# Kernel tuning notes

Measured on AMD Instinct MI355X. Metric: run time of the kernel, lower is better.

The kernel has to match this reference:

```python
import jax, jax.numpy as jnp
import numpy as np

N_HEAD = 16    # config.n_head
T_STEPS = 3    # config.T: PC energy-minimization steps
LR = 0.01      # config.local_learning_rate


def _causal_attention(x, Wq, Wk, Wv):
    # x: [B, S, E] latent activity; generative model f(x) = causal MHA(x)
    B, S, E = x.shape
    D = E // N_HEAD
    def split(h):  # [B,S,E] -> [B,H,S,D]
        return h.reshape(B, S, N_HEAD, D).transpose(0, 2, 1, 3)
    q = split(x @ Wq.T)
    k = split(x @ Wk.T)
    v = split(x @ Wv.T)
    scores = jnp.einsum('bhqd,bhkd->bhqk', q, k) / jnp.sqrt(jnp.asarray(D, x.dtype))
    mask = jnp.tril(jnp.ones((S, S), dtype=bool))
    scores = jnp.where(mask, scores, jnp.asarray(-1e30, x.dtype))
    att = jax.nn.softmax(scores, axis=-1)
    out = jnp.einsum('bhqk,bhkd->bhqd', att, v)
    return out.transpose(0, 2, 1, 3).reshape(B, S, E)


def _pc_infer(target, f):
    # PCLayer: T steps of gradient descent on E(x) = 0.5 * ||target - f(x)||^2
    # x_init = 'zeros'; returns the inferred latent x (PCLayer.get_x).
    x = jnp.zeros_like(target)
    energy = lambda z: 0.5 * jnp.sum((target - f(z)) ** 2)
    g = jax.grad(energy)
    for _ in range(T_STEPS):  # fixed small T: unrolled
        x = x - LR * g(x)
    return x


def setup_inputs() -> dict:
    key = jax.random.key(0)
    ks = jax.random.split(key, 5)
    B, S, E = 2, 1024, 1024
    fc1_x = jax.random.normal(ks[0], (B, S, E), dtype=jnp.float32)
    init = lambda k: 0.02 * jax.random.normal(k, (E, E), dtype=jnp.float32)
    return {
        'fc1_x': fc1_x,
        'Wq': init(ks[1]),
        'Wk': init(ks[2]),
        'Wv': init(ks[3]),
        'Wo': init(ks[4]),
    }


def reference(fc1_x, Wq, Wk, Wv, Wo):
    # Stage 1 (pc_output): infer pre-output latent att_score s.t. output-proj
    # Wo @ att_score ~ fc1_x  (generative model f1(x) = x @ Wo^T, bias=False).
    att_score = _pc_infer(fc1_x, lambda z: z @ Wo.T)
    # Stage 2 (pc_qkv): infer latent x_qkv s.t. causal MHA(x_qkv) ~ att_score.
    x_qkv = _pc_infer(att_score, lambda z: _causal_attention(z, Wq, Wk, Wv))
    return x_qkv
```

## Files before the change

kernel.cpp:

```cpp
#include <hip/hip_runtime.h>
#include <hip/hip_bf16.h>
#include <math.h>

#define S_LEN 1024
#define E_DIM 1024
#define NH 16
#define HD 64
#define M_ROWS 2048
#define BH_CNT 32

static constexpr float LR_C = 0.01f;
static constexpr float SC_C = 0.125f;
static constexpr float C2_C = 0.125f * 1.44269504f;

typedef unsigned short ushort_t;
typedef __attribute__((ext_vector_type(8))) __bf16 bf16x8;
typedef __attribute__((ext_vector_type(4))) float f32x4;

static __device__ inline ushort_t f2bu(float f) {
  __hip_bfloat16 h = __float2bfloat16(f);
  return *(ushort_t*)&h;
}
static __device__ inline bf16x8 ldg8(const ushort_t* p) { return *(const bf16x8*)p; }

static __device__ inline void async_cp16(const ushort_t* g, __bf16* lds_wave_base) {
  __builtin_amdgcn_global_load_lds((const __attribute__((address_space(1))) void*)g,
                                   (__attribute__((address_space(3))) void*)lds_wave_base,
                                   16, 0, 0);
}

static __device__ inline void stage_tile(const ushort_t* src, size_t src_stride,
                                         ushort_t* lds, int lane, int wave) {
  int rl = lane >> 3;
  int c = ((lane & 7) - rl) & 7;
  #pragma unroll
  for (int t = 0; t < 2; t++) {
    int s = wave * 2 + t;
    async_cp16(src + (size_t)(s * 8 + rl) * src_stride + c * 8,
               (__bf16*)(lds + s * 512));
  }
}
static __device__ inline const bf16x8* tile_at(const ushort_t* lds, int r, int cchunk) {
  return (const bf16x8*)(lds + r * 64 + (((cchunk + r) & 7) * 8));
}

__global__ __launch_bounds__(256) void prep_w4(
    const float* __restrict__ Wo, const float* __restrict__ Wq,
    const float* __restrict__ Wk, const float* __restrict__ Wv,
    ushort_t* __restrict__ o0, ushort_t* __restrict__ t0,
    ushort_t* __restrict__ o1, ushort_t* __restrict__ t1,
    ushort_t* __restrict__ o2, ushort_t* __restrict__ t2,
    ushort_t* __restrict__ o3, ushort_t* __restrict__ t3) {
  __shared__ float ts[64][65];
  int z = blockIdx.z;
  const float* W = (z == 0) ? Wo : (z == 1) ? Wq : (z == 2) ? Wk : Wv;
  ushort_t* Wb  = (z == 0) ? o0 : (z == 1) ? o1 : (z == 2) ? o2 : o3;
  ushort_t* WTb = (z == 0) ? t0 : (z == 1) ? t1 : (z == 2) ? t2 : t3;
  int bx = blockIdx.x * 64, by = blockIdx.y * 64;
  int t = threadIdx.x;
  int rr = t >> 6, cc = t & 63;
  #pragma unroll
  for (int p = 0; p < 16; p++) {
    int r = p * 4 + rr;
    float v = W[(size_t)(by + r) * E_DIM + bx + cc];
    ts[r][cc] = v;
    Wb[(size_t)(by + r) * E_DIM + bx + cc] = f2bu(v);
  }
  __syncthreads();
  #pragma unroll
  for (int p = 0; p < 16; p++) {
    int r = p * 4 + rr;
    WTb[(size_t)(bx + r) * E_DIM + by + cc] = f2bu(ts[cc][r]);
  }
}

__global__ __launch_bounds__(256) void k_cast(const float* __restrict__ in,
                                              ushort_t* __restrict__ out, int n4) {
  int i = blockIdx.x * 256 + threadIdx.x;
  if (i < n4) {
    float4 v = ((const float4*)in)[i];
    ushort_t p[4] = {f2bu(v.x), f2bu(v.y), f2bu(v.z), f2bu(v.w)};
    *(uint2*)(out + (size_t)i * 4) = *(uint2*)p;
  }
}

__global__ __launch_bounds__(256) void k_scan1(const float* __restrict__ Xs,
                                               float* __restrict__ Sf,
                                               float* __restrict__ tot) {
  int e = blockIdx.x * 256 + threadIdx.x;
  int b = blockIdx.y;
  int z = blockIdx.z;
  float acc = 0.f;
  for (int i = z * 64 + 63; i >= z * 64; i--) {
    size_t idx = ((size_t)b * S_LEN + i) * E_DIM + e;
    acc = fmaf(Xs[idx], 1.0f / (float)(i + 1), acc);
    Sf[idx] = acc;
  }
  tot[((size_t)b * 16 + z) * E_DIM + e] = acc;
}

__global__ __launch_bounds__(256) void k_scan2(const float* __restrict__ Sf,
                                               const float* __restrict__ tot,
                                               ushort_t* __restrict__ Sb) {
  int e = blockIdx.x * 256 + threadIdx.x;
  int b = blockIdx.y;
  int z = blockIdx.z;
  float off = 0.f;
  for (int c = z + 1; c < 16; c++) off += tot[((size_t)b * 16 + c) * E_DIM + e];
  for (int i = z * 64; i < z * 64 + 64; i++) {
    size_t idx = ((size_t)b * S_LEN + i) * E_DIM + e;
    Sb[idx] = f2bu(Sf[idx] + off);
  }
}

template <int MODE>
__global__ __launch_bounds__(256) void gemm_mf(
    const ushort_t* __restrict__ A, const ushort_t* __restrict__ B,
    float* __restrict__ Cf, ushort_t* __restrict__ Cb0, float alpha) {
  const int K = 1024;
  __shared__ __bf16 As[2][2][64][32];
  __shared__ __bf16 Bs[2][2][64][32];
  int tid = threadIdx.x;
  int m0 = blockIdx.y * 64, n0 = blockIdx.x * 64;

  int lane = tid & 63, wave = tid >> 6;
  int wrow = wave >> 1, wcol = wave & 1;
  int fr = lane & 15, q = lane >> 4;

  int srow = wave * 16 + (lane >> 2);
  int scg = ((lane & 3) + (srow >> 1)) & 3;
  int scol = scg * 8;

  int rA0 = wrow * 32 + fr, rA1r = rA0 + 16;
  int rB0 = wcol * 32 + fr, rB1r = rB0 + 16;
  int cA0 = ((q - (rA0 >> 1)) & 3) * 8;
  int cA1 = ((q - (rA1r >> 1)) & 3) * 8;
  int cB0 = ((q - (rB0 >> 1)) & 3) * 8;
  int cB1 = ((q - (rB1r >> 1)) & 3) * 8;

  const ushort_t* ga = A + (size_t)(m0 + srow) * K + scol;
  const ushort_t* gb = B + (size_t)(n0 + srow) * K + scol;

  f32x4 acc[2][2] = {};

  async_cp16(ga,      &As[0][0][wave * 16][0]);
  async_cp16(ga + 32, &As[0][1][wave * 16][0]);
  async_cp16(gb,      &Bs[0][0][wave * 16][0]);
  async_cp16(gb + 32, &Bs[0][1][wave * 16][0]);

  #pragma unroll 1
  for (int k0 = 0; k0 < K; k0 += 64) {
    int cur = (k0 >> 6) & 1;
    __syncthreads();
    if (k0 + 64 < K) {
      int nxt = cur ^ 1;
      async_cp16(ga + k0 + 64, &As[nxt][0][wave * 16][0]);
      async_cp16(ga + k0 + 96, &As[nxt][1][wave * 16][0]);
      async_cp16(gb + k0 + 64, &Bs[nxt][0][wave * 16][0]);
      async_cp16(gb + k0 + 96, &Bs[nxt][1][wave * 16][0]);
    }
    bf16x8 a00 = *(const bf16x8*)&As[cur][0][rA0][cA0];
    bf16x8 a01 = *(const bf16x8*)&As[cur][1][rA0][cA0];
    bf16x8 a10 = *(const bf16x8*)&As[cur][0][rA1r][cA1];
    bf16x8 a11 = *(const bf16x8*)&As[cur][1][rA1r][cA1];
    bf16x8 b00 = *(const bf16x8*)&Bs[cur][0][rB0][cB0];
    bf16x8 b01 = *(const bf16x8*)&Bs[cur][1][rB0][cB0];
    bf16x8 b10 = *(const bf16x8*)&Bs[cur][0][rB1r][cB1];
    bf16x8 b11 = *(const bf16x8*)&Bs[cur][1][rB1r][cB1];
    acc[0][0] = __builtin_amdgcn_mfma_f32_16x16x32_bf16(a00, b00, acc[0][0], 0, 0, 0);
    acc[0][1] = __builtin_amdgcn_mfma_f32_16x16x32_bf16(a00, b10, acc[0][1], 0, 0, 0);
    acc[1][0] = __builtin_amdgcn_mfma_f32_16x16x32_bf16(a10, b00, acc[1][0], 0, 0, 0);
    acc[1][1] = __builtin_amdgcn_mfma_f32_16x16x32_bf16(a10, b10, acc[1][1], 0, 0, 0);
    acc[0][0] = __builtin_amdgcn_mfma_f32_16x16x32_bf16(a01, b01, acc[0][0], 0, 0, 0);
    acc[0][1] = __builtin_amdgcn_mfma_f32_16x16x32_bf16(a01, b11, acc[0][1], 0, 0, 0);
    acc[1][0] = __builtin_amdgcn_mfma_f32_16x16x32_bf16(a11, b01, acc[1][0], 0, 0, 0);
    acc[1][1] = __builtin_amdgcn_mfma_f32_16x16x32_bf16(a11, b11, acc[1][1], 0, 0, 0);
  }

  #pragma unroll
  for (int mi = 0; mi < 2; mi++)
    #pragma unroll
    for (int ni = 0; ni < 2; ni++) {
      int col = n0 + wcol * 32 + ni * 16 + fr;
      int row0 = m0 + wrow * 32 + mi * 16 + q * 4;
      #pragma unroll
      for (int r = 0; r < 4; r++) {
        size_t idx = (size_t)(row0 + r) * E_DIM + col;
        float v = acc[mi][ni][r];
        if (MODE == 3) {
          Cf[idx] = v;
        } else if (MODE == 4) {
          Cf[idx] = v;
          Cb0[idx] = f2bu(v);
        } else if (MODE == 6) {
          float nv = alpha * v;
          Cf[idx] = nv;
          Cb0[idx] = f2bu(nv);
        } else if (MODE == 7) {
          float nv = -3.f * LR_C * LR_C * Cf[idx] + LR_C * LR_C * LR_C * v;
          if (row0 + r == col) nv += 3.f * LR_C;
          Cb0[idx] = f2bu(nv);
        } else {
          Cb0[idx] = f2bu(v);
        }
      }
    }
}

__global__ __launch_bounds__(256) void gemm_qkv(
    const ushort_t* __restrict__ A,
    const ushort_t* __restrict__ B0, const ushort_t* __restrict__ B1, const ushort_t* __restrict__ B2,
    ushort_t* __restrict__ Cb0, ushort_t* __restrict__ Cb1, ushort_t* __restrict__ Cb2,
    ushort_t* __restrict__ Ct0, ushort_t* __restrict__ Ct1, ushort_t* __restrict__ Ct2) {
  const int K = 1024;
  __shared__ __bf16 As[2][2][64][32];
  __shared__ __bf16 Bs[2][3][2][64][32];
  int tid = threadIdx.x;
  int m0 = blockIdx.y * 64, n0 = blockIdx.x * 64;

  int lane = tid & 63, wave = tid >> 6;
  int wrow = wave >> 1, wcol = wave & 1;
  int fr = lane & 15, q = lane >> 4;

  int srow = wave * 16 + (lane >> 2);
  int scg = ((lane & 3) + (srow >> 1)) & 3;
  int scol = scg * 8;

  int rA0 = wrow * 32 + fr, rA1r = rA0 + 16;
  int rB0 = wcol * 32 + fr, rB1r = rB0 + 16;
  int cA0 = ((q - (rA0 >> 1)) & 3) * 8;
  int cA1 = ((q - (rA1r >> 1)) & 3) * 8;
  int cB0 = ((q - (rB0 >> 1)) & 3) * 8;
  int cB1 = ((q - (rB1r >> 1)) & 3) * 8;

  const ushort_t* ga = A + (size_t)(m0 + srow) * K + scol;
  const ushort_t* gb0 = B0 + (size_t)(n0 + srow) * K + scol;
  const ushort_t* gb1 = B1 + (size_t)(n0 + srow) * K + scol;
  const ushort_t* gb2 = B2 + (size_t)(n0 + srow) * K + scol;

  f32x4 acc[3][2][2] = {};

  async_cp16(ga,       &As[0][0][wave * 16][0]);
  async_cp16(ga + 32,  &As[0][1][wave * 16][0]);
  async_cp16(gb0,      &Bs[0][0][0][wave * 16][0]);
  async_cp16(gb0 + 32, &Bs[0][0][1][wave * 16][0]);
  async_cp16(gb1,      &Bs[0][1][0][wave * 16][0]);
  async_cp16(gb1 + 32, &Bs[0][1][1][wave * 16][0]);
  async_cp16(gb2,      &Bs[0][2][0][wave * 16][0]);
  async_cp16(gb2 + 32, &Bs[0][2][1][wave * 16][0]);

  #pragma unroll 1
  for (int k0 = 0; k0 < K; k0 += 64) {
    int cur = (k0 >> 6) & 1;
    __syncthreads();
    if (k0 + 64 < K) {
      int nxt = cur ^ 1;
      async_cp16(ga + k0 + 64,  &As[nxt][0][wave * 16][0]);
      async_cp16(ga + k0 + 96,  &As[nxt][1][wave * 16][0]);
      async_cp16(gb0 + k0 + 64, &Bs[nxt][0][0][wave * 16][0]);
      async_cp16(gb0 + k0 + 96, &Bs[nxt][0][1][wave * 16][0]);
      async_cp16(gb1 + k0 + 64, &Bs[nxt][1][0][wave * 16][0]);
      async_cp16(gb1 + k0 + 96, &Bs[nxt][1][1][wave * 16][0]);
      async_cp16(gb2 + k0 + 64, &Bs[nxt][2][0][wave * 16][0]);
      async_cp16(gb2 + k0 + 96, &Bs[nxt][2][1][wave * 16][0]);
    }
    bf16x8 a00 = *(const bf16x8*)&As[cur][0][rA0][cA0];
    bf16x8 a01 = *(const bf16x8*)&As[cur][1][rA0][cA0];
    bf16x8 a10 = *(const bf16x8*)&As[cur][0][rA1r][cA1];
    bf16x8 a11 = *(const bf16x8*)&As[cur][1][rA1r][cA1];
    #pragma unroll
    for (int z = 0; z < 3; z++) {
      bf16x8 b00 = *(const bf16x8*)&Bs[cur][z][0][rB0][cB0];
      bf16x8 b01 = *(const bf16x8*)&Bs[cur][z][1][rB0][cB0];
      bf16x8 b10 = *(const bf16x8*)&Bs[cur][z][0][rB1r][cB1];
      bf16x8 b11 = *(const bf16x8*)&Bs[cur][z][1][rB1r][cB1];
      acc[z][0][0] = __builtin_amdgcn_mfma_f32_16x16x32_bf16(a00, b00, acc[z][0][0], 0, 0, 0);
      acc[z][0][1] = __builtin_amdgcn_mfma_f32_16x16x32_bf16(a00, b10, acc[z][0][1], 0, 0, 0);
      acc[z][1][0] = __builtin_amdgcn_mfma_f32_16x16x32_bf16(a10, b00, acc[z][1][0], 0, 0, 0);
      acc[z][1][1] = __builtin_amdgcn_mfma_f32_16x16x32_bf16(a10, b10, acc[z][1][1], 0, 0, 0);
      acc[z][0][0] = __builtin_amdgcn_mfma_f32_16x16x32_bf16(a01, b01, acc[z][0][0], 0, 0, 0);
      acc[z][0][1] = __builtin_amdgcn_mfma_f32_16x16x32_bf16(a01, b11, acc[z][0][1], 0, 0, 0);
      acc[z][1][0] = __builtin_amdgcn_mfma_f32_16x16x32_bf16(a11, b01, acc[z][1][0], 0, 0, 0);
      acc[z][1][1] = __builtin_amdgcn_mfma_f32_16x16x32_bf16(a11, b11, acc[z][1][1], 0, 0, 0);
    }
  }

  #pragma unroll
  for (int z = 0; z < 3; z++) {
    ushort_t* Cbz = (z == 0) ? Cb0 : (z == 1) ? Cb1 : Cb2;
    ushort_t* Ctz = (z == 0) ? Ct0 : (z == 1) ? Ct1 : Ct2;
    float tsc = (z == 2) ? 1.0f : SC_C;
    #pragma unroll
    for (int mi = 0; mi < 2; mi++)
      #pragma unroll
      for (int ni = 0; ni < 2; ni++) {
        int col = n0 + wcol * 32 + ni * 16 + fr;
        int row0 = m0 + wrow * 32 + mi * 16 + q * 4;
        ushort_t pk[4];
        #pragma unroll
        for (int r = 0; r < 4; r++) {
          size_t idx = (size_t)(row0 + r) * E_DIM + col;
          float v = acc[z][mi][ni][r];
          Cbz[idx] = f2bu(v);
          pk[r] = f2bu(v * tsc);
        }
        int hh = col >> 6, dd = col & 63;
        int bb = row0 >> 10, ss = row0 & 1023;
        *(uint2*)(Ctz + ((size_t)((bb * NH + hh) * HD + dd)) * S_LEN + ss) = *(uint2*)pk;
      }
  }
}

__global__ __launch_bounds__(256) void gemm_acc(
    const ushort_t* __restrict__ A0, const ushort_t* __restrict__ A1, const ushort_t* __restrict__ A2,
    const ushort_t* __restrict__ B0, const ushort_t* __restrict__ B1, const ushort_t* __restrict__ B2,
    float* __restrict__ Cf, ushort_t* __restrict__ Cb, float alpha) {
  const int K = 1024;
  __shared__ __bf16 As[3][2][64][32];
  __shared__ __bf16 Bs[3][2][64][32];
  int tid = threadIdx.x;
  int m0 = blockIdx.y * 64, n0 = blockIdx.x * 64;

  int lane = tid & 63, wave = tid >> 6;
  int wrow = wave >> 1, wcol = wave & 1;
  int fr = lane & 15, q = lane >> 4;

  int srow = wave * 16 + (lane >> 2);
  int scg = ((lane & 3) + (srow >> 1)) & 3;
  int scol = scg * 8;

  int rA0 = wrow * 32 + fr, rA1r = rA0 + 16;
  int rB0 = wcol * 32 + fr, rB1r = rB0 + 16;
  int cA0 = ((q - (rA0 >> 1)) & 3) * 8;
  int cA1 = ((q - (rA1r >> 1)) & 3) * 8;
  int cB0 = ((q - (rB0 >> 1)) & 3) * 8;
  int cB1 = ((q - (rB1r >> 1)) & 3) * 8;

  f32x4 acc[3][2][2] = {};

  const ushort_t* ga0 = A0 + (size_t)(m0 + srow) * K + scol;
  const ushort_t* ga1 = A1 + (size_t)(m0 + srow) * K + scol;
  const ushort_t* ga2 = A2 + (size_t)(m0 + srow) * K + scol;
  const ushort_t* gb0 = B0 + (size_t)(n0 + srow) * K + scol;
  const ushort_t* gb1 = B1 + (size_t)(n0 + srow) * K + scol;
  const ushort_t* gb2 = B2 + (size_t)(n0 + srow) * K + scol;

  #pragma unroll 1
  for (int k0 = 0; k0 < K; k0 += 64) {
    __syncthreads();
    async_cp16(ga0 + k0,      &As[0][0][wave * 16][0]);
    async_cp16(ga0 + k0 + 32, &As[0][1][wave * 16][0]);
    async_cp16(ga1 + k0,      &As[1][0][wave * 16][0]);
    async_cp16(ga1 + k0 + 32, &As[1][1][wave * 16][0]);
    async_cp16(ga2 + k0,      &As[2][0][wave * 16][0]);
    async_cp16(ga2 + k0 + 32, &As[2][1][wave * 16][0]);
    async_cp16(gb0 + k0,      &Bs[0][0][wave * 16][0]);
    async_cp16(gb0 + k0 + 32, &Bs[0][1][wave * 16][0]);
    async_cp16(gb1 + k0,      &Bs[1][0][wave * 16][0]);
    async_cp16(gb1 + k0 + 32, &Bs[1][1][wave * 16][0]);
    async_cp16(gb2 + k0,      &Bs[2][0][wave * 16][0]);
    async_cp16(gb2 + k0 + 32, &Bs[2][1][wave * 16][0]);
    __syncthreads();
    #pragma unroll
    for (int z = 0; z < 3; z++) {
      bf16x8 a00 = *(const bf16x8*)&As[z][0][rA0][cA0];
      bf16x8 a01 = *(const bf16x8*)&As[z][1][rA0][cA0];
      bf16x8 a10 = *(const bf16x8*)&As[z][0][rA1r][cA1];
      bf16x8 a11 = *(const bf16x8*)&As[z][1][rA1r][cA1];
      bf16x8 b00 = *(const bf16x8*)&Bs[z][0][rB0][cB0];
      bf16x8 b01 = *(const bf16x8*)&Bs[z][1][rB0][cB0];
      bf16x8 b10 = *(const bf16x8*)&Bs[z][0][rB1r][cB1];
      bf16x8 b11 = *(const bf16x8*)&Bs[z][1][rB1r][cB1];
      acc[z][0][0] = __builtin_amdgcn_mfma_f32_16x16x32_bf16(a00, b00, acc[z][0][0], 0, 0, 0);
      acc[z][0][1] = __builtin_amdgcn_mfma_f32_16x16x32_bf16(a00, b10, acc[z][0][1], 0, 0, 0);
      acc[z][1][0] = __builtin_amdgcn_mfma_f32_16x16x32_bf16(a10, b00, acc[z][1][0], 0, 0, 0);
      acc[z][1][1] = __builtin_amdgcn_mfma_f32_16x16x32_bf16(a10, b10, acc[z][1][1], 0, 0, 0);
      acc[z][0][0] = __builtin_amdgcn_mfma_f32_16x16x32_bf16(a01, b01, acc[z][0][0], 0, 0, 0);
      acc[z][0][1] = __builtin_amdgcn_mfma_f32_16x16x32_bf16(a01, b11, acc[z][0][1], 0, 0, 0);
      acc[z][1][0] = __builtin_amdgcn_mfma_f32_16x16x32_bf16(a11, b01, acc[z][1][0], 0, 0, 0);
      acc[z][1][1] = __builtin_amdgcn_mfma_f32_16x16x32_bf16(a11, b11, acc[z][1][1], 0, 0, 0);
    }
  }

  #pragma unroll
  for (int mi = 0; mi < 2; mi++)
    #pragma unroll
    for (int ni = 0; ni < 2; ni++) {
      int col = n0 + wcol * 32 + ni * 16 + fr;
      int row0 = m0 + wrow * 32 + mi * 16 + q * 4;
      #pragma unroll
      for (int r = 0; r < 4; r++) {
        size_t idx = (size_t)(row0 + r) * E_DIM + col;
        float v = (acc[0][mi][ni][r] + acc[1][mi][ni][r]) + acc[2][mi][ni][r];
        float nv = Cf[idx] + alpha * v;
        Cf[idx] = nv;
        Cb[idx] = f2bu(nv);
      }
    }
}


__global__ __launch_bounds__(256) void fwd_fused(const ushort_t* __restrict__ Qg,
                                                 const ushort_t* __restrict__ Kg,
                                                 const ushort_t* __restrict__ Vt,
                                                 const float* __restrict__ Xs,
                                                 float* __restrict__ mbuf,
                                                 ushort_t* __restrict__ Gb,
                                                 ushort_t* __restrict__ Gt,
                                                 float* __restrict__ Dv) {
  int bh = blockIdx.x, y = blockIdx.y;
  int it = (y < 8) ? (15 - y) : (y - 8);
  int b = bh >> 4, h = bh & 15;
  int tid = threadIdx.x, lane = tid & 63, wv = tid >> 6;
  int fr = lane & 15, q = lane >> 4;
  int i0 = it * 64, band = wv * 16;
  __shared__ ushort_t Ksb[2][4096];
  __shared__ ushort_t Vsb[2][4096];
  __shared__ ushort_t Ps[64][72];

  const ushort_t* Kbase = Kg + (size_t)(b * S_LEN) * E_DIM + h * HD;
  const ushort_t* Vbase = Vt + (size_t)(bh * HD) * S_LEN;

  const ushort_t* Qrow = Qg + (size_t)(b * S_LEN + i0 + band + fr) * E_DIM + h * HD;
  bf16x8 aq0 = ldg8(Qrow + q * 8);
  bf16x8 aq1 = ldg8(Qrow + 32 + q * 8);

  float m[4], l[4];
  #pragma unroll
  for (int r = 0; r < 4; r++) { m[r] = -1e30f; l[r] = 0.f; }
  f32x4 oacc[4] = {};

  stage_tile(Kbase, E_DIM, Ksb[0], lane, wv);
  stage_tile(Vbase, S_LEN, Vsb[0], lane, wv);

  #pragma unroll 1
  for (int jt = 0; jt <= it; jt++) {
    int j0 = jt * 64;
    int cur = jt & 1;
    __syncthreads();
    if (jt < it) {
      int j0n = j0 + 64;
      stage_tile(Kbase + (size_t)j0n * E_DIM, E_DIM, Ksb[cur ^ 1], lane, wv);
      stage_tile(Vbase + j0n, S_LEN, Vsb[cur ^ 1], lane, wv);
    }
    const ushort_t* Ks = Ksb[cur];
    const ushort_t* Vs = Vsb[cur];
    f32x4 sA[4];
    #pragma unroll
    for (int nc = 0; nc < 4; nc++) {
      bf16x8 bk0 = *tile_at(Ks, nc * 16 + fr, q);
      bf16x8 bk1 = *tile_at(Ks, nc * 16 + fr, q + 4);
      f32x4 z = {};
      z = __builtin_amdgcn_mfma_f32_16x16x32_bf16(aq0, bk0, z, 0, 0, 0);
      sA[nc] = __builtin_amdgcn_mfma_f32_16x16x32_bf16(aq1, bk1, z, 0, 0, 0);
    }
    float sv[4][4];
    if (jt == it) {
      #pragma unroll
      for (int nc = 0; nc < 4; nc++)
        #pragma unroll
        for (int r = 0; r < 4; r++) {
          int row = i0 + band + q * 4 + r;
          int col = j0 + nc * 16 + fr;
          sv[nc][r] = (col <= row) ? sA[nc][r] * C2_C : -1e30f;
        }
    } else {
      #pragma unroll
      for (int nc = 0; nc < 4; nc++)
        #pragma unroll
        for (int r = 0; r < 4; r++)
          sv[nc][r] = sA[nc][r] * C2_C;
    }
    #pragma unroll
    for (int r = 0; r < 4; r++) {
      float mx = fmaxf(fmaxf(sv[0][r], sv[1][r]), fmaxf(sv[2][r], sv[3][r]));
      #pragma unroll
      for (int off = 1; off < 16; off <<= 1) mx = fmaxf(mx, __shfl_xor(mx, off, 64));
      float mn = fmaxf(m[r], mx);
      float alpha = exp2f(m[r] - mn);
      float ps = 0.f;
      #pragma unroll
      for (int nc = 0; nc < 4; nc++) {
        float p = exp2f(sv[nc][r] - mn);
        Ps[band + q * 4 + r][nc * 16 + fr] = f2bu(p);
        ps += p;
      }
      l[r] = l[r] * alpha + ps;
      m[r] = mn;
      #pragma unroll
      for (int nc = 0; nc < 4; nc++) oacc[nc][r] *= alpha;
    }
    bf16x8 ap0 = *(const bf16x8*)&Ps[band + fr][q * 8];
    bf16x8 ap1 = *(const bf16x8*)&Ps[band + fr][32 + q * 8];
    #pragma unroll
    for (int nc = 0; nc < 4; nc++) {
      bf16x8 bv0 = *tile_at(Vs, nc * 16 + fr, q);
      bf16x8 bv1 = *tile_at(Vs, nc * 16 + fr, q + 4);
      oacc[nc] = __builtin_amdgcn_mfma_f32_16x16x32_bf16(ap0, bv0, oacc[nc], 0, 0, 0);
      oacc[nc] = __builtin_amdgcn_mfma_f32_16x16x32_bf16(ap1, bv1, oacc[nc], 0, 0, 0);
    }
  }
  #pragma unroll
  for (int r = 0; r < 4; r++) {
    #pragma unroll
    for (int off = 1; off < 16; off <<= 1) l[r] += __shfl_xor(l[r], off, 64);
  }
  float linv[4];
  #pragma unroll
  for (int r = 0; r < 4; r++) linv[r] = 1.0f / l[r];
  float dpart[4] = {};
  #pragma unroll
  for (int nc = 0; nc < 4; nc++) {
    ushort_t pg[4];
    #pragma unroll
    for (int r = 0; r < 4; r++) {
      int row = i0 + band + q * 4 + r;
      size_t gi = (size_t)(b * S_LEN + row) * E_DIM + h * HD + nc * 16 + fr;
      float o = oacc[nc][r] * linv[r];
      float g = o - Xs[gi];
      ushort_t bu = f2bu(g);
      Gb[gi] = bu;
      pg[r] = bu;
      dpart[r] += g * o;
    }
    int d = nc * 16 + fr;
    int s0 = i0 + band + q * 4;
    *(uint2*)(Gt + ((size_t)bh * HD + d) * S_LEN + s0) = *(uint2*)pg;
  }
  #pragma unroll
  for (int r = 0; r < 4; r++) {
    #pragma unroll
    for (int off = 1; off < 16; off <<= 1) dpart[r] += __shfl_xor(dpart[r], off, 64);
  }
  if (fr == 0) {
    #pragma unroll
    for (int r = 0; r < 4; r++) {
      size_t sid = (size_t)bh * S_LEN + i0 + band + q * 4 + r;
      mbuf[sid] = m[r] + log2f(l[r]);
      Dv[sid] = dpart[r];
    }
  }
}

__global__ __launch_bounds__(256) void bwd_fused(const ushort_t* __restrict__ Qg,
                                                 const ushort_t* __restrict__ Kg,
                                                 const ushort_t* __restrict__ Vg,
                                                 const ushort_t* __restrict__ Gg,
                                                 const ushort_t* __restrict__ Qt,
                                                 const ushort_t* __restrict__ Kt,
                                                 const ushort_t* __restrict__ Gt,
                                                 const float* __restrict__ mbuf,
                                                 const float* __restrict__ Dv,
                                                 ushort_t* __restrict__ GQ,
                                                 ushort_t* __restrict__ GK,
                                                 ushort_t* __restrict__ GV) {
  int bh = blockIdx.x, y = blockIdx.y;
  int b = bh >> 4, h = bh & 15;
  int tid = threadIdx.x, lane = tid & 63, wv = tid >> 6;
  int fr = lane & 15, q = lane >> 4;
  int band = wv * 16;
  __shared__ ushort_t tA[4][4096];
  __shared__ ushort_t tP[2][64][72];

  {
    ushort_t* Ks = tA[0];
    ushort_t* Vs = tA[1];
    ushort_t* Ts = tA[2];
    ushort_t (*dSs)[72] = tP[0];
    int it = y, i0 = it * 64;

    const ushort_t* KbaseA = Kg + (size_t)(b * S_LEN) * E_DIM + h * HD;
    const ushort_t* VbaseA = Vg + (size_t)(b * S_LEN) * E_DIM + h * HD;
    const ushort_t* TbaseA = Kt + (size_t)(bh * HD) * S_LEN;

    const ushort_t* Qrow = Qg + (size_t)(b * S_LEN + i0 + band + fr) * E_DIM + h * HD;
    const ushort_t* Grow = Gg + (size_t)(b * S_LEN + i0 + band + fr) * E_DIM + h * HD;
    bf16x8 aq0 = ldg8(Qrow + q * 8), aq1 = ldg8(Qrow + 32 + q * 8);
    bf16x8 ag0 = ldg8(Grow + q * 8), ag1 = ldg8(Grow + 32 + q * 8);

    float mrow[4], Dr[4];
    #pragma unroll
    for (int r = 0; r < 4; r++) {
      size_t sid = (size_t)bh * S_LEN + i0 + band + q * 4 + r;
      mrow[r] = mbuf[sid]; Dr[r] = Dv[sid];
    }
    f32x4 dqacc[4] = {};

    #pragma unroll 1
    for (int jt = 0; jt <= it; jt++) {
      int j0 = jt * 64;
      __syncthreads();
      stage_tile(KbaseA + (size_t)j0 * E_DIM, E_DIM, Ks, lane, wv);
      stage_tile(VbaseA + (size_t)j0 * E_DIM, E_DIM, Vs, lane, wv);
      stage_tile(TbaseA + j0, S_LEN, Ts, lane, wv);
      __syncthreads();
      f32x4 sA[4], dpA[4];
      #pragma unroll
      for (int nc = 0; nc < 4; nc++) {
        bf16x8 bk0 = *tile_at(Ks, nc * 16 + fr, q);
        bf16x8 bk1 = *tile_at(Ks, nc * 16 + fr, q + 4);
        bf16x8 bv0 = *tile_at(Vs, nc * 16 + fr, q);
        bf16x8 bv1 = *tile_at(Vs, nc * 16 + fr, q + 4);
        f32x4 z = {};
        z = __builtin_amdgcn_mfma_f32_16x16x32_bf16(aq0, bk0, z, 0, 0, 0);
        sA[nc] = __builtin_amdgcn_mfma_f32_16x16x32_bf16(aq1, bk1, z, 0, 0, 0);
        f32x4 z2 = {};
        z2 = __builtin_amdgcn_mfma_f32_16x16x32_bf16(ag0, bv0, z2, 0, 0, 0);
        dpA[nc] = __builtin_amdgcn_mfma_f32_16x16x32_bf16(ag1, bv1, z2, 0, 0, 0);
      }
      if (jt == it) {
        #pragma unroll
        for (int nc = 0; nc < 4; nc++)
          #pragma unroll
          for (int r = 0; r < 4; r++) {
            int row = i0 + band + q * 4 + r;
            int col = j0 + nc * 16 + fr;
            float ds = 0.f;
            if (col <= row) {
              float P = exp2f(fmaf(sA[nc][r], C2_C, -mrow[r]));
              ds = P * (dpA[nc][r] - Dr[r]);
            }
            dSs[band + q * 4 + r][nc * 16 + fr] = f2bu(ds);
          }
      } else {
        #pragma unroll
        for (int nc = 0; nc < 4; nc++)
          #pragma unroll
          for (int r = 0; r < 4; r++) {
            float P = exp2f(fmaf(sA[nc][r], C2_C, -mrow[r]));
            float ds = P * (dpA[nc][r] - Dr[r]);
            dSs[band + q * 4 + r][nc * 16 + fr] = f2bu(ds);
          }
      }
      bf16x8 ad0 = *(const bf16x8*)&dSs[band + fr][q * 8];
      bf16x8 ad1 = *(const bf16x8*)&dSs[band + fr][32 + q * 8];
      #pragma unroll
      for (int nc = 0; nc < 4; nc++) {
        bf16x8 bt0 = *tile_at(Ts, nc * 16 + fr, q);
        bf16x8 bt1 = *tile_at(Ts, nc * 16 + fr, q + 4);
        dqacc[nc] = __builtin_amdgcn_mfma_f32_16x16x32_bf16(ad0, bt0, dqacc[nc], 0, 0, 0);
        dqacc[nc] = __builtin_amdgcn_mfma_f32_16x16x32_bf16(ad1, bt1, dqacc[nc], 0, 0, 0);
      }
    }
    #pragma unroll
    for (int nc = 0; nc < 4; nc++)
      #pragma unroll
      for (int r = 0; r < 4; r++) {
        int row = i0 + band + q * 4 + r;
        size_t gi = (size_t)(b * S_LEN + row) * E_DIM + h * HD + nc * 16 + fr;
        GQ[gi] = f2bu(dqacc[nc][r]);
      }
  }

  {
    ushort_t* Qs  = tA[0];
    ushort_t* Gs  = tA[1];
    ushort_t* Qts = tA[2];
    ushort_t* Gts = tA[3];
    ushort_t (*PT)[72]  = tP[0];
    ushort_t (*dST)[72] = tP[1];
    int jt = y, j0 = jt * 64;

    const ushort_t* QbaseB = Qg + (size_t)(b * S_LEN) * E_DIM + h * HD;
    const ushort_t* GbaseB = Gg + (size_t)(b * S_LEN) * E_DIM + h * HD;
    const ushort_t* QtbaseB = Qt + (size_t)(bh * HD) * S_LEN;
    const ushort_t* GtbaseB = Gt + (size_t)(bh * HD) * S_LEN;

    const ushort_t* Krow = Kg + (size_t)(b * S_LEN + j0 + band + fr) * E_DIM + h * HD;
    const ushort_t* Vrow = Vg + (size_t)(b * S_LEN + j0 + band + fr) * E_DIM + h * HD;
    bf16x8 ak0 = ldg8(Krow + q * 8), ak1 = ldg8(Krow + 32 + q * 8);
    bf16x8 av0 = ldg8(Vrow + q * 8), av1 = ldg8(Vrow + 32 + q * 8);

    f32x4 dkacc[4] = {}, dvacc[4] = {};

    #pragma unroll 1
    for (int i_t = jt; i_t < 16; i_t++) {
      int i0 = i_t * 64;
      __syncthreads();
      stage_tile(QbaseB + (size_t)i0 * E_DIM, E_DIM, Qs, lane, wv);
      stage_tile(GbaseB + (size_t)i0 * E_DIM, E_DIM, Gs, lane, wv);
      stage_tile(QtbaseB + i0, S_LEN, Qts, lane, wv);
      stage_tile(GtbaseB + i0, S_LEN, Gts, lane, wv);
      __syncthreads();
      float mc[4], Dc[4];
      #pragma unroll
      for (int nc = 0; nc < 4; nc++) {
        size_t sid = (size_t)bh * S_LEN + i0 + nc * 16 + fr;
        mc[nc] = mbuf[sid]; Dc[nc] = Dv[sid];
      }
      f32x4 stA[4], dptA[4];
      #pragma unroll
      for (int nc = 0; nc < 4; nc++) {
        bf16x8 bq0 = *tile_at(Qs, nc * 16 + fr, q);
        bf16x8 bq1 = *tile_at(Qs, nc * 16 + fr, q + 4);
        bf16x8 bg0 = *tile_at(Gs, nc * 16 + fr, q);
        bf16x8 bg1 = *tile_at(Gs, nc * 16 + fr, q + 4);
        f32x4 z = {};
        z = __builtin_amdgcn_mfma_f32_16x16x32_bf16(ak0, bq0, z, 0, 0, 0);
        stA[nc] = __builtin_amdgcn_mfma_f32_16x16x32_bf16(ak1, bq1, z, 0, 0, 0);
        f32x4 z2 = {};
        z2 = __builtin_amdgcn_mfma_f32_16x16x32_bf16(av0, bg0, z2, 0, 0, 0);
        dptA[nc] = __builtin_amdgcn_mfma_f32_16x16x32_bf16(av1, bg1, z2, 0, 0, 0);
      }
      if (i_t == jt) {
        #pragma unroll
        for (int nc = 0; nc < 4; nc++)
          #pragma unroll
          for (int r = 0; r < 4; r++) {
            int jrow = j0 + band + q * 4 + r;
            int icol = i0 + nc * 16 + fr;
            float P = 0.f, ds = 0.f;
            if (icol >= jrow) {
              P = exp2f(fmaf(stA[nc][r], C2_C, -mc[nc]));
              ds = P * (dptA[nc][r] - Dc[nc]);
            }
            PT[band + q * 4 + r][nc * 16 + fr] = f2bu(P);
            dST[band + q * 4 + r][nc * 16 + fr] = f2bu(ds);
          }
      } else {
        #pragma unroll
        for (int nc = 0; nc < 4; nc++)
          #pragma unroll
          for (int r = 0; r < 4; r++) {
            float P = exp2f(fmaf(stA[nc][r], C2_C, -mc[nc]));
            float ds = P * (dptA[nc][r] - Dc[nc]);
            PT[band + q * 4 + r][nc * 16 + fr] = f2bu(P);
            dST[band + q * 4 + r][nc * 16 + fr] = f2bu(ds);
          }
      }
      bf16x8 ap0 = *(const bf16x8*)&PT[band + fr][q * 8];
      bf16x8 ap1 = *(const bf16x8*)&PT[band + fr][32 + q * 8];
      bf16x8 ad0 = *(const bf16x8*)&dST[band + fr][q * 8];
      bf16x8 ad1 = *(const bf16x8*)&dST[band + fr][32 + q * 8];
      #pragma unroll
      for (int nc = 0; nc < 4; nc++) {
        bf16x8 bg0 = *tile_at(Gts, nc * 16 + fr, q);
        bf16x8 bg1 = *tile_at(Gts, nc * 16 + fr, q + 4);
        bf16x8 bq0 = *tile_at(Qts, nc * 16 + fr, q);
        bf16x8 bq1 = *tile_at(Qts, nc * 16 + fr, q + 4);
        dvacc[nc] = __builtin_amdgcn_mfma_f32_16x16x32_bf16(ap0, bg0, dvacc[nc], 0, 0, 0);
        dvacc[nc] = __builtin_amdgcn_mfma_f32_16x16x32_bf16(ap1, bg1, dvacc[nc], 0, 0, 0);
        dkacc[nc] = __builtin_amdgcn_mfma_f32_16x16x32_bf16(ad0, bq0, dkacc[nc], 0, 0, 0);
        dkacc[nc] = __builtin_amdgcn_mfma_f32_16x16x32_bf16(ad1, bq1, dkacc[nc], 0, 0, 0);
      }
    }
    #pragma unroll
    for (int nc = 0; nc < 4; nc++)
      #pragma unroll
      for (int r = 0; r < 4; r++) {
        int jrow = j0 + band + q * 4 + r;
        size_t gi = (size_t)(b * S_LEN + jrow) * E_DIM + h * HD + nc * 16 + fr;
        GK[gi] = f2bu(dkacc[nc][r]);
        GV[gi] = f2bu(dvacc[nc][r]);
      }
  }
}

extern "C" void kernel_launch(void* const* d_in, const int* in_sizes, int n_in,
                              void* d_out, int out_size, void* d_ws, size_t ws_size,
                              hipStream_t stream) {
  const float* T1 = (const float*)d_in[0];
  const float* Wq = (const float*)d_in[1];
  const float* Wk = (const float*)d_in[2];
  const float* Wv = (const float*)d_in[3];
  const float* Wo = (const float*)d_in[4];

  const size_t M2 = 2097152;
  const size_t M1 = 1048576;
  float* w = (float*)d_ws;
  float* Xs = w;
  float* mS = Xs + M2;
  float* DvS = mS + 65536;
  ushort_t* u = (ushort_t*)(DvS + 65536);
  ushort_t* W0 = u;          ushort_t* W1 = W0 + M1;  ushort_t* W2 = W1 + M1;
  ushort_t* W3 = W2 + M1;    ushort_t* W4 = W3 + M1;  ushort_t* W5 = W4 + M1;
  ushort_t* Qb = W5 + M1;    ushort_t* Kb = Qb + M2;  ushort_t* Vb = Kb + M2;
  ushort_t* Qt = Vb + M2;    ushort_t* Kt = Qt + M2;  ushort_t* Vt = Kt + M2;
  ushort_t* Gt = Vt + M2;
  ushort_t* Gb = Gt + M2;
  ushort_t* GQb = Gb + M2;   ushort_t* GKb = GQb + M2; ushort_t* GVb = GKb + M2;
  ushort_t* X2b = GVb + M2;
  float* X2 = (float*)d_out;

  ushort_t* WoB = Gb;
  ushort_t* WoT = Gt;
  float* Mf  = (float*)Qb;
  ushort_t* Mb  = Vt;
  ushort_t* Nb  = Vb;
  ushort_t* AtB = Qt;
  ushort_t* T1b = Kt;

  float* Sf  = (float*)GQb;
  float* tot = mS;
  ushort_t* Sb = GVb;

  dim3 p4grid(16, 16, 4);
  dim3 sgrid(16, 16);
  dim3 ggrid(16, 32);
  dim3 agrid(BH_CNT, 16);

  prep_w4<<<p4grid, 256, 0, stream>>>(Wo, Wq, Wk, Wv,
                                      WoB, WoT, W0, W3, W1, W4, W2, W5);
  k_cast<<<(M2 / 4 + 255) / 256, 256, 0, stream>>>(T1, T1b, (int)(M2 / 4));
  gemm_mf<4><<<sgrid, 256, 0, stream>>>(WoT, WoT, Mf, Mb, 0.f);
  gemm_mf<7><<<sgrid, 256, 0, stream>>>(Mb, Mb, Mf, Nb, 0.f);
  gemm_mf<5><<<sgrid, 256, 0, stream>>>(Nb, WoB, nullptr, AtB, 0.f);
  gemm_mf<3><<<ggrid, 256, 0, stream>>>(T1b, AtB, Xs, nullptr, 0.f);

  k_scan1<<<dim3(E_DIM / 256, 2, 16), 256, 0, stream>>>(Xs, Sf, tot);
  k_scan2<<<dim3(E_DIM / 256, 2, 16), 256, 0, stream>>>(Sf, tot, Sb);
  gemm_mf<6><<<ggrid, 256, 0, stream>>>(Sb, W5, X2, X2b, LR_C);

  for (int t = 1; t < 3; t++) {
    gemm_qkv<<<ggrid, 256, 0, stream>>>(X2b, W0, W1, W2,
                                        Qb, Kb, Vb, Qt, Kt, Vt);
    fwd_fused<<<agrid, 256, 0, stream>>>(Qb, Kb, Vt, Xs, mS, Gb, Gt, DvS);
    bwd_fused<<<agrid, 256, 0, stream>>>(Qb, Kb, Vb, Gb, Qt, Kt, Gt, mS, DvS,
                                         GQb, GKb, GVb);
    gemm_acc<<<ggrid, 256, 0, stream>>>(GQb, GKb, GVb, W3, W4, W5,
                                        X2, X2b, -LR_C);
  }
}
```

Baseline: 389.6 us.

## Double-buffer gemm_acc over a flattened 48-stage loop with a single accumulator

```diff
diff --git a/kernel.cpp b/kernel.cpp
--- a/kernel.cpp
+++ b/kernel.cpp
@@ -316,8 +316,8 @@
     const ushort_t* __restrict__ B0, const ushort_t* __restrict__ B1, const ushort_t* __restrict__ B2,
     float* __restrict__ Cf, ushort_t* __restrict__ Cb, float alpha) {
   const int K = 1024;
-  __shared__ __bf16 As[3][2][64][32];
-  __shared__ __bf16 Bs[3][2][64][32];
+  __shared__ __bf16 As[2][2][64][32];
+  __shared__ __bf16 Bs[2][2][64][32];
   int tid = threadIdx.x;
   int m0 = blockIdx.y * 64, n0 = blockIdx.x * 64;
 
@@ -336,8 +336,6 @@
   int cB0 = ((q - (rB0 >> 1)) & 3) * 8;
   int cB1 = ((q - (rB1r >> 1)) & 3) * 8;
 
-  f32x4 acc[3][2][2] = {};
-
   const ushort_t* ga0 = A0 + (size_t)(m0 + srow) * K + scol;
   const ushort_t* ga1 = A1 + (size_t)(m0 + srow) * K + scol;
   const ushort_t* ga2 = A2 + (size_t)(m0 + srow) * K + scol;
@@ -345,41 +343,45 @@
   const ushort_t* gb1 = B1 + (size_t)(n0 + srow) * K + scol;
   const ushort_t* gb2 = B2 + (size_t)(n0 + srow) * K + scol;
 
+  f32x4 acc[2][2] = {};
+
+  async_cp16(ga0,      &As[0][0][wave * 16][0]);
+  async_cp16(ga0 + 32, &As[0][1][wave * 16][0]);
+  async_cp16(gb0,      &Bs[0][0][wave * 16][0]);
+  async_cp16(gb0 + 32, &Bs[0][1][wave * 16][0]);
+
   #pragma unroll 1
-  for (int k0 = 0; k0 < K; k0 += 64) {
+  for (int s = 0; s < 48; s++) {
+    int cur = s & 1;
     __syncthreads();
-    async_cp16(ga0 + k0,      &As[0][0][wave * 16][0]);
-    async_cp16(ga0 + k0 + 32, &As[0][1][wave * 16][0]);
-    async_cp16(ga1 + k0,      &As[1][0][wave * 16][0]);
-    async_cp16(ga1 + k0 + 32, &As[1][1][wave * 16][0]);
-    async_cp16(ga2 + k0,      &As[2][0][wave * 16][0]);
-    async_cp16(ga2 + k0 + 32, &As[2][1][wave * 16][0]);
-    async_cp16(gb0 + k0,      &Bs[0][0][wave * 16][0]);
-    async_cp16(gb0 + k0 + 32, &Bs[0][1][wave * 16][0]);
-    async_cp16(gb1 + k0,      &Bs[1][0][wave * 16][0]);
-    async_cp16(gb1 + k0 + 32, &Bs[1][1][wave * 16][0]);
-    async_cp16(gb2 + k0,      &Bs[2][0][wave * 16][0]);
-    async_cp16(gb2 + k0 + 32, &Bs[2][1][wave * 16][0]);
-    __syncthreads();
-    #pragma unroll
-    for (int z = 0; z < 3; z++) {
-      bf16x8 a00 = *(const bf16x8*)&As[z][0][rA0][cA0];
-      bf16x8 a01 = *(const bf16x8*)&As[z][1][rA0][cA0];
-      bf16x8 a10 = *(const bf16x8*)&As[z][0][rA1r][cA1];
-      bf16x8 a11 = *(const bf16x8*)&As[z][1][rA1r][cA1];
-      bf16x8 b00 = *(const bf16x8*)&Bs[z][0][rB0][cB0];
-      bf16x8 b01 = *(const bf16x8*)&Bs[z][1][rB0][cB0];
-      bf16x8 b10 = *(const bf16x8*)&Bs[z][0][rB1r][cB1];
-      bf16x8 b11 = *(const bf16x8*)&Bs[z][1][rB1r][cB1];
-      acc[z][0][0] = __builtin_amdgcn_mfma_f32_16x16x32_bf16(a00, b00, acc[z][0][0], 0, 0, 0);
-      acc[z][0][1] = __builtin_amdgcn_mfma_f32_16x16x32_bf16(a00, b10, acc[z][0][1], 0, 0, 0);
-      acc[z][1][0] = __builtin_amdgcn_mfma_f32_16x16x32_bf16(a10, b00, acc[z][1][0], 0, 0, 0);
-      acc[z][1][1] = __builtin_amdgcn_mfma_f32_16x16x32_bf16(a10, b10, acc[z][1][1], 0, 0, 0);
-      acc[z][0][0] = __builtin_amdgcn_mfma_f32_16x16x32_bf16(a01, b01, acc[z][0][0], 0, 0, 0);
-      acc[z][0][1] = __builtin_amdgcn_mfma_f32_16x16x32_bf16(a01, b11, acc[z][0][1], 0, 0, 0);
-      acc[z][1][0] = __builtin_amdgcn_mfma_f32_16x16x32_bf16(a11, b01, acc[z][1][0], 0, 0, 0);
-      acc[z][1][1] = __builtin_amdgcn_mfma_f32_16x16x32_bf16(a11, b11, acc[z][1][1], 0, 0, 0);
-    }
+    if (s + 1 < 48) {
+      int sn = s + 1;
+      int segn = sn >> 4;
+      int kn = (sn & 15) << 6;
+      const ushort_t* gan = (segn == 0) ? ga0 : (segn == 1) ? ga1 : ga2;
+      const ushort_t* gbn = (segn == 0) ? gb0 : (segn == 1) ? gb1 : gb2;
+      int nxt = cur ^ 1;
+      async_cp16(gan + kn,      &As[nxt][0][wave * 16][0]);
+      async_cp16(gan + kn + 32, &As[nxt][1][wave * 16][0]);
+      async_cp16(gbn + kn,      &Bs[nxt][0][wave * 16][0]);
+      async_cp16(gbn + kn + 32, &Bs[nxt][1][wave * 16][0]);
+    }
+    bf16x8 a00 = *(const bf16x8*)&As[cur][0][rA0][cA0];
+    bf16x8 a01 = *(const bf16x8*)&As[cur][1][rA0][cA0];
+    bf16x8 a10 = *(const bf16x8*)&As[cur][0][rA1r][cA1];
+    bf16x8 a11 = *(const bf16x8*)&As[cur][1][rA1r][cA1];
+    bf16x8 b00 = *(const bf16x8*)&Bs[cur][0][rB0][cB0];
+    bf16x8 b01 = *(const bf16x8*)&Bs[cur][1][rB0][cB0];
+    bf16x8 b10 = *(const bf16x8*)&Bs[cur][0][rB1r][cB1];
+    bf16x8 b11 = *(const bf16x8*)&Bs[cur][1][rB1r][cB1];
+    acc[0][0] = __builtin_amdgcn_mfma_f32_16x16x32_bf16(a00, b00, acc[0][0], 0, 0, 0);
+    acc[0][1] = __builtin_amdgcn_mfma_f32_16x16x32_bf16(a00, b10, acc[0][1], 0, 0, 0);
+    acc[1][0] = __builtin_amdgcn_mfma_f32_16x16x32_bf16(a10, b00, acc[1][0], 0, 0, 0);
+    acc[1][1] = __builtin_amdgcn_mfma_f32_16x16x32_bf16(a10, b10, acc[1][1], 0, 0, 0);
+    acc[0][0] = __builtin_amdgcn_mfma_f32_16x16x32_bf16(a01, b01, acc[0][0], 0, 0, 0);
+    acc[0][1] = __builtin_amdgcn_mfma_f32_16x16x32_bf16(a01, b11, acc[0][1], 0, 0, 0);
+    acc[1][0] = __builtin_amdgcn_mfma_f32_16x16x32_bf16(a11, b01, acc[1][0], 0, 0, 0);
+    acc[1][1] = __builtin_amdgcn_mfma_f32_16x16x32_bf16(a11, b11, acc[1][1], 0, 0, 0);
   }
 
   #pragma unroll
@@ -391,8 +393,7 @@
       #pragma unroll
       for (int r = 0; r < 4; r++) {
         size_t idx = (size_t)(row0 + r) * E_DIM + col;
-        float v = (acc[0][mi][ni][r] + acc[1][mi][ni][r]) + acc[2][mi][ni][r];
-        float nv = Cf[idx] + alpha * v;
+        float nv = Cf[idx] + alpha * acc[mi][ni][r];
         Cf[idx] = nv;
         Cb[idx] = f2bu(nv);
       }
```

Measured after the change: 412.6 us. 5.9% more time.
